# Kernel optimization log

Measured on AMD Instinct MI355X. Metric: run time of the kernel, lower is better.

Reference implementation:

```python
import jax, jax.numpy as jnp
import numpy as np

N = 160000   # total nodes
G = 800      # total graphs (B * 50)
NPG = 200    # nodes per graph
E = 1280000  # total edges (avg degree 8)
B = 16       # proteins
K = 2        # TAGConv hops
IN_F = 31
HID = 64


def setup_inputs() -> dict:
    key = jax.random.key(0)
    ks = jax.random.split(key, 16)
    s = 0.1
    x = jax.random.normal(ks[0], (N, IN_F), jnp.float32)
    src = jax.random.randint(ks[1], (E,), 0, N, jnp.int32)
    dst = jax.random.randint(ks[2], (E,), 0, N, jnp.int32)
    node2graph = jnp.repeat(jnp.arange(G, dtype=jnp.int32), NPG)
    W0 = jax.random.normal(ks[3], (IN_F * (K + 1), HID), jnp.float32) * s
    b0 = jax.random.normal(ks[4], (HID,), jnp.float32) * s
    W1 = jax.random.normal(ks[5], (HID * (K + 1), HID), jnp.float32) * s
    b1 = jax.random.normal(ks[6], (HID,), jnp.float32) * s
    W2 = jax.random.normal(ks[7], (HID * (K + 1), HID), jnp.float32) * s
    b2 = jax.random.normal(ks[8], (HID,), jnp.float32) * s
    W3 = jax.random.normal(ks[9], (HID * (K + 1), HID), jnp.float32) * s
    b3 = jax.random.normal(ks[10], (HID,), jnp.float32) * s
    Wg = jax.random.normal(ks[11], (HID, 1), jnp.float32) * s
    bg = jax.random.normal(ks[12], (1,), jnp.float32) * s
    return dict(x=x, src=src, dst=dst, node2graph=node2graph,
                W0=W0, b0=b0, W1=W1, b1=b1, W2=W2, b2=b2, W3=W3, b3=b3,
                Wg=Wg, bg=bg)


def reference(x, src, dst, node2graph, W0, b0, W1, b1, W2, b2, W3, b3, Wg, bg):
    # symmetric normalization: norm = in_degree^{-1/2}, clamped at 1 (DGL TAGConv)
    deg = jax.ops.segment_sum(jnp.ones((E,), x.dtype), dst, num_segments=N)
    norm = jax.lax.rsqrt(jnp.clip(deg, 1.0))[:, None]  # [N,1]

    def tag_conv(h, W, b):
        hops = [h]
        for _ in range(K):
            h = norm * jax.ops.segment_sum((h * norm)[src], dst, num_segments=N)
            hops.append(h)
        return jnp.concatenate(hops, axis=-1) @ W + b

    h = x
    for W, b in ((W0, b0), (W1, b1), (W2, b2), (W3, b3)):
        h = jax.nn.relu(tag_conv(h, W, b))

    # GlobalAttentionPooling: per-graph softmax over gate logits, weighted sum
    gate = h @ Wg + bg  # [N,1]
    gmax = jax.ops.segment_max(gate, node2graph, num_segments=G)  # [G,1]
    e = jnp.exp(gate - gmax[node2graph])
    z = jax.ops.segment_sum(e, node2graph, num_segments=G)
    alpha = e / z[node2graph]
    readout = jax.ops.segment_sum(alpha * h, node2graph, num_segments=G)  # [G,64]
    return readout.reshape(B, 50, HID)
```

## Files before the change

### kernel.cpp

```cpp
#include <hip/hip_runtime.h>

#define NN 160000
#define NE 1280000
#define NG 800
#define NPGR 200
#define INF_ 31
#define HID 64

#define NBUK 256
#define NPBK 625
#define BCAP 6144
#define CHUNK 8192

typedef unsigned short bfu;
typedef __attribute__((ext_vector_type(8))) short short8;
typedef __attribute__((ext_vector_type(4))) float f32x4;

__device__ inline float bflo(unsigned u) { return __uint_as_float(u << 16); }
__device__ inline float bfhi(unsigned u) { return __uint_as_float(u & 0xffff0000u); }
__device__ inline float bfs(bfu s) { return __uint_as_float(((unsigned)s) << 16); }
__device__ inline unsigned f2bf(float x) {
  unsigned u = __float_as_uint(x);
  return (u + 0x7fffu + ((u >> 16) & 1u)) >> 16;
}
__device__ inline unsigned pack2(float a, float b) {
  return f2bf(a) | (f2bf(b) << 16);
}
__device__ inline void unpack8(uint4 v, float* f) {
  f[0] = bflo(v.x); f[1] = bfhi(v.x);
  f[2] = bflo(v.y); f[3] = bfhi(v.y);
  f[4] = bflo(v.z); f[5] = bfhi(v.z);
  f[6] = bflo(v.w); f[7] = bfhi(v.w);
}

__global__ __launch_bounds__(256) void k_pad(const float* __restrict__ x,
                                             bfu* __restrict__ xb) {
  int i = blockIdx.x * 256 + threadIdx.x;
  int n = i >> 5, f = i & 31;
  float v = (f < INF_) ? x[(size_t)n * INF_ + f] : 0.f;
  xb[i] = (bfu)f2bf(v);
}

__global__ __launch_bounds__(256) void k_wfrag(const float* __restrict__ W,
                                               short* __restrict__ Wf) {
  int idx = blockIdx.x * 256 + threadIdx.x;
  int lane = idx & 63, t = (idx >> 6) & 3, step = idx >> 8;
  int col = t * 16 + (lane & 15);
  int kbase = step * 32 + ((lane >> 4) & 3) * 8;
  short8 o;
#pragma unroll
  for (int j = 0; j < 8; ++j)
    o[j] = (short)f2bf(W[(size_t)(kbase + j) * 64 + col]);
  *reinterpret_cast<short8*>(&Wf[(size_t)idx * 8]) = o;
}

__global__ __launch_bounds__(256) void k_wfrag0(const float* __restrict__ W0,
                                                short* __restrict__ Wf) {
  int idx = blockIdx.x * 256 + threadIdx.x;
  int lane = idx & 63, t = (idx >> 6) & 3, step = idx >> 8;
  int col = t * 16 + (lane & 15);
  int kbase = step * 32 + ((lane >> 4) & 3) * 8;
  short8 o;
#pragma unroll
  for (int j = 0; j < 8; ++j) {
    int r = kbase + j, pp = r >> 5, ir = r & 31;
    float v = (ir < INF_) ? W0[(size_t)(pp * INF_ + ir) * 64 + col] : 0.f;
    o[j] = (short)f2bf(v);
  }
  *reinterpret_cast<short8*>(&Wf[(size_t)idx * 8]) = o;
}

__global__ __launch_bounds__(256) void k_gcinit(int* __restrict__ gcur) {
  gcur[threadIdx.x] = threadIdx.x * BCAP;
}

__global__ __launch_bounds__(256) void k_bucket(const int* __restrict__ src,
    const int* __restrict__ dst, int* __restrict__ gcur,
    uint2* __restrict__ buk, int E) {
  __shared__ uint2 stage[CHUNK];
  __shared__ int cnt[NBUK], gbase[NBUK];
  int tid = threadIdx.x;
  int base = blockIdx.x * CHUNK;
  int nch = min(CHUNK, E - base);
  for (int i = tid; i < NBUK; i += 256) cnt[i] = 0;
  __syncthreads();
  for (int i = tid * 4; i < nch; i += 1024) {
    int4 s4 = *reinterpret_cast<const int4*>(&src[base + i]);
    int4 d4 = *reinterpret_cast<const int4*>(&dst[base + i]);
    stage[i + 0] = make_uint2((unsigned)s4.x, (unsigned)d4.x);
    stage[i + 1] = make_uint2((unsigned)s4.y, (unsigned)d4.y);
    stage[i + 2] = make_uint2((unsigned)s4.z, (unsigned)d4.z);
    stage[i + 3] = make_uint2((unsigned)s4.w, (unsigned)d4.w);
    atomicAdd(&cnt[(unsigned)d4.x / NPBK], 1);
    atomicAdd(&cnt[(unsigned)d4.y / NPBK], 1);
    atomicAdd(&cnt[(unsigned)d4.z / NPBK], 1);
    atomicAdd(&cnt[(unsigned)d4.w / NPBK], 1);
  }
  __syncthreads();
  for (int i = tid; i < NBUK; i += 256) {
    gbase[i] = atomicAdd(&gcur[i], cnt[i]);
    cnt[i] = 0;
  }
  __syncthreads();
  for (int i = tid; i < nch; i += 256) {
    uint2 r = stage[i];
    int b = r.y / NPBK;
    int off = atomicAdd(&cnt[b], 1);
    buk[(size_t)gbase[b] + off] = r;
  }
}

__global__ __launch_bounds__(256) void k_count(const uint2* __restrict__ buk,
    const int* __restrict__ gcur, int* __restrict__ deg,
    int* __restrict__ order) {
  __shared__ int cnt[NPBK];
  __shared__ int h64[64], c64[64];
  int b = blockIdx.x, tid = threadIdx.x;
  int nbase = b * NPBK;
  for (int i = tid; i < NPBK; i += 256) cnt[i] = 0;
  if (tid < 64) h64[tid] = 0;
  __syncthreads();
  int n = gcur[b] - b * BCAP;
  const uint2* __restrict__ bp = buk + (size_t)b * BCAP;
  for (int i = tid; i < n; i += 256) atomicAdd(&cnt[bp[i].y - nbase], 1);
  __syncthreads();
  for (int i = tid; i < NPBK; i += 256) {
    int c = cnt[i];
    deg[nbase + i] = c;
    atomicAdd(&h64[min(c, 63)], 1);
  }
  __syncthreads();
  if (tid == 0) {
    int s = 0;
    for (int k = 0; k < 64; ++k) { c64[k] = s; s += h64[k]; }
  }
  __syncthreads();
  for (int i = tid; i < NPBK; i += 256) {
    int pos = atomicAdd(&c64[min(cnt[i], 63)], 1);
    order[nbase + pos] = nbase + i;
  }
}

__global__ __launch_bounds__(256) void k_bscan(const int* __restrict__ gcur,
                                               int* __restrict__ bktoff) {
  __shared__ int sh[256];
  int tid = threadIdx.x;
  sh[tid] = gcur[tid] - tid * BCAP;
  __syncthreads();
  for (int off = 1; off < 256; off <<= 1) {
    int v = (tid >= off) ? sh[tid - off] : 0;
    __syncthreads();
    sh[tid] += v;
    __syncthreads();
  }
  bktoff[tid] = (tid > 0) ? sh[tid - 1] : 0;
}

__global__ __launch_bounds__(256) void k_scat2(const uint2* __restrict__ buk,
    const int* __restrict__ gcur, const int* __restrict__ bktoff,
    const int* __restrict__ deg, int* __restrict__ rp,
    unsigned* __restrict__ csr) {
  __shared__ int cur[NPBK];
  __shared__ int psum[256];
  int b = blockIdx.x, tid = threadIdx.x;
  int nbase = b * NPBK;
  int i0 = tid * 3;
  int d0 = (i0 + 0 < NPBK) ? deg[nbase + i0 + 0] : 0;
  int d1 = (i0 + 1 < NPBK) ? deg[nbase + i0 + 1] : 0;
  int d2 = (i0 + 2 < NPBK) ? deg[nbase + i0 + 2] : 0;
  psum[tid] = d0 + d1 + d2;
  __syncthreads();
  for (int off = 1; off < 256; off <<= 1) {
    int v = (tid >= off) ? psum[tid - off] : 0;
    __syncthreads();
    psum[tid] += v;
    __syncthreads();
  }
  int excl = bktoff[b] + ((tid > 0) ? psum[tid - 1] : 0);
  if (i0 + 0 < NPBK) { cur[i0 + 0] = excl; rp[nbase + i0 + 0] = excl; excl += d0; }
  if (i0 + 1 < NPBK) { cur[i0 + 1] = excl; rp[nbase + i0 + 1] = excl; excl += d1; }
  if (i0 + 2 < NPBK) { cur[i0 + 2] = excl; rp[nbase + i0 + 2] = excl; excl += d2; }
  if (b == NBUK - 1 && tid == 0) rp[NN] = NE;
  __syncthreads();
  int n = gcur[b] - b * BCAP;
  const uint2* __restrict__ bp = buk + (size_t)b * BCAP;
  for (int i = tid; i < n; i += 256) {
    uint2 r = bp[i];
    int pos = atomicAdd(&cur[r.y - nbase], 1);
    unsigned d = min((unsigned)deg[r.x], 16383u);
    csr[pos] = (d << 18) | r.x;
  }
}

template<int F>
__device__ inline uint4 gather_node(const bfu* __restrict__ hin,
    const unsigned* __restrict__ csr, int beg, int end, int f8) {
  float acc[8] = {0.f, 0.f, 0.f, 0.f, 0.f, 0.f, 0.f, 0.f};
  int e = beg;
  for (; e + 8 <= end; e += 8) {
    unsigned ed[8];
    uint4 v[8];
#pragma unroll
    for (int k = 0; k < 8; ++k) ed[k] = csr[e + k];
#pragma unroll
    for (int k = 0; k < 8; ++k)
      v[k] = *reinterpret_cast<const uint4*>(&hin[(size_t)(ed[k] & 0x3FFFFu) * F + f8]);
#pragma unroll
    for (int k = 0; k < 8; ++k) {
      float f[8];
      unpack8(v[k], f);
      float w = rsqrtf(fmaxf((float)(ed[k] >> 18), 1.0f));
#pragma unroll
      for (int q = 0; q < 8; ++q) acc[q] = fmaf(f[q], w, acc[q]);
    }
  }
  for (; e + 2 <= end; e += 2) {
    unsigned e0 = csr[e], e1 = csr[e + 1];
    uint4 v0 = *reinterpret_cast<const uint4*>(&hin[(size_t)(e0 & 0x3FFFFu) * F + f8]);
    uint4 v1 = *reinterpret_cast<const uint4*>(&hin[(size_t)(e1 & 0x3FFFFu) * F + f8]);
    float f0[8], f1[8];
    unpack8(v0, f0); unpack8(v1, f1);
    float w0 = rsqrtf(fmaxf((float)(e0 >> 18), 1.0f));
    float w1 = rsqrtf(fmaxf((float)(e1 >> 18), 1.0f));
#pragma unroll
    for (int q = 0; q < 8; ++q) {
      acc[q] = fmaf(f0[q], w0, acc[q]);
      acc[q] = fmaf(f1[q], w1, acc[q]);
    }
  }
  if (e < end) {
    unsigned e0 = csr[e];
    uint4 v0 = *reinterpret_cast<const uint4*>(&hin[(size_t)(e0 & 0x3FFFFu) * F + f8]);
    float f0[8];
    unpack8(v0, f0);
    float w0 = rsqrtf(fmaxf((float)(e0 >> 18), 1.0f));
#pragma unroll
    for (int q = 0; q < 8; ++q) acc[q] = fmaf(f0[q], w0, acc[q]);
  }
  float wn = rsqrtf(fmaxf((float)(end - beg), 1.0f));
#pragma unroll
  for (int q = 0; q < 8; ++q) acc[q] *= wn;
  uint4 o;
  o.x = pack2(acc[0], acc[1]);
  o.y = pack2(acc[2], acc[3]);
  o.z = pack2(acc[4], acc[5]);
  o.w = pack2(acc[6], acc[7]);
  return o;
}

template<int F>
__global__ __launch_bounds__(256) void k_gather(const bfu* __restrict__ hin,
    const int* __restrict__ rp, const unsigned* __restrict__ csr,
    const int* __restrict__ order, bfu* __restrict__ hout) {
  constexpr int LPN = F / 8;
  constexpr int NPB = 256 / LPN;
  int slot = threadIdx.x / LPN;
  int f8 = (threadIdx.x % LPN) * 8;
  int nid = order[blockIdx.x * NPB + slot];
  int beg = rp[nid], end = rp[nid + 1];
  uint4 o = gather_node<F>(hin, csr, beg, end, f8);
  *reinterpret_cast<uint4*>(&hout[(size_t)nid * F + f8]) = o;
}

template<int F>
__global__ __launch_bounds__(256) void k_hop2gemm(const bfu* __restrict__ h0,
    const bfu* __restrict__ h1, const int* __restrict__ rp,
    const unsigned* __restrict__ csr, const int* __restrict__ order,
    const short* __restrict__ Wf, const float* __restrict__ bias,
    bfu* __restrict__ outb) {
  constexpr int SPP = F / 32;
  constexpr int LPN = F / 8;
  constexpr int NPR = 256 / LPN;
  constexpr int NFB = F / 8;
  __shared__ uint4 hs[64 * (NFB + 1)];

  int tid = threadIdx.x;
  int nb = blockIdx.x * 64;

#pragma unroll
  for (int round = 0; round < 64 / NPR; ++round) {
    int slot = round * NPR + tid / LPN;
    int f8 = tid % LPN;
    int nid = order[nb + slot];
    int beg = rp[nid], end = rp[nid + 1];
    uint4 o = gather_node<F>(h1, csr, beg, end, f8 * 8);
    hs[slot * (NFB + 1) + f8] = o;
  }
  __syncthreads();

  int wave = tid >> 6, lane = tid & 63;
  int quad = lane >> 4, l15 = lane & 15;
  int aslot = wave * 16 + l15;
  int anid = order[nb + aslot];

  f32x4 acc[4] = {{0.f,0.f,0.f,0.f}, {0.f,0.f,0.f,0.f},
                  {0.f,0.f,0.f,0.f}, {0.f,0.f,0.f,0.f}};
  const bfu* parts[2] = {h0, h1};
#pragma unroll
  for (int p = 0; p < 2; ++p) {
    const bfu* __restrict__ P = parts[p] + (size_t)anid * F + quad * 8;
#pragma unroll
    for (int s = 0; s < SPP; ++s) {
      short8 a = *reinterpret_cast<const short8*>(P + s * 32);
      int step = p * SPP + s;
      const short* __restrict__ wb = Wf + ((size_t)step * 4 * 64 + lane) * 8;
#pragma unroll
      for (int t = 0; t < 4; ++t) {
        short8 b = *reinterpret_cast<const short8*>(wb + (size_t)t * 64 * 8);
        acc[t] = __builtin_amdgcn_mfma_f32_16x16x32_bf16(a, b, acc[t], 0, 0, 0);
      }
    }
  }
#pragma unroll
  for (int s = 0; s < SPP; ++s) {
    short8 a = *reinterpret_cast<const short8*>(&hs[aslot * (NFB + 1) + s * 4 + quad]);
    int step = 2 * SPP + s;
    const short* __restrict__ wb = Wf + ((size_t)step * 4 * 64 + lane) * 8;
#pragma unroll
    for (int t = 0; t < 4; ++t) {
      short8 b = *reinterpret_cast<const short8*>(wb + (size_t)t * 64 * 8);
      acc[t] = __builtin_amdgcn_mfma_f32_16x16x32_bf16(a, b, acc[t], 0, 0, 0);
    }
  }
#pragma unroll
  for (int t = 0; t < 4; ++t) {
    int col = t * 16 + l15;
    float bj = bias[col];
#pragma unroll
    for (int r = 0; r < 4; ++r) {
      int node = order[nb + wave * 16 + quad * 4 + r];
      float v = fmaxf(acc[t][r] + bj, 0.f);
      outb[(size_t)node * 64 + col] = (bfu)f2bf(v);
    }
  }
}

__global__ __launch_bounds__(256) void k_pool(const bfu* __restrict__ h,
    const float* __restrict__ Wg, const float* __restrict__ bg,
    float* __restrict__ out) {
  __shared__ uint4 hsl[NPGR * 8];
  __shared__ float sgate[NPGR];
  __shared__ float sred[256];
  __shared__ float spart[4][64];
  int g = blockIdx.x;
  int tid = threadIdx.x;
  int lane = tid & 63, w = tid >> 6;
  const uint4* __restrict__ hg4 = reinterpret_cast<const uint4*>(
      h + (size_t)g * NPGR * HID);
  for (int i = tid; i < NPGR * 8; i += 256) hsl[i] = hg4[i];
  __syncthreads();
  const bfu* hsb = reinterpret_cast<const bfu*>(hsl);
  float wgt = Wg[lane];

  for (int n = w; n < NPGR; n += 4) {
    float v = bfs(hsb[n * HID + lane]) * wgt;
    for (int off = 32; off > 0; off >>= 1) v += __shfl_down(v, off, 64);
    if (lane == 0) sgate[n] = v + bg[0];
  }
  __syncthreads();

  float m = -INFINITY;
  for (int n = tid; n < NPGR; n += 256) m = fmaxf(m, sgate[n]);
  sred[tid] = m;
  __syncthreads();
  for (int s = 128; s > 0; s >>= 1) {
    if (tid < s) sred[tid] = fmaxf(sred[tid], sred[tid + s]);
    __syncthreads();
  }
  float gmax = sred[0];
  __syncthreads();

  float zp = 0.f;
  for (int n = tid; n < NPGR; n += 256) {
    float e = expf(sgate[n] - gmax);
    sgate[n] = e;
    zp += e;
  }
  sred[tid] = zp;
  __syncthreads();
  for (int s = 128; s > 0; s >>= 1) {
    if (tid < s) sred[tid] += sred[tid + s];
    __syncthreads();
  }
  float z = sred[0];
  __syncthreads();

  float acc = 0.f;
  for (int n = w; n < NPGR; n += 4)
    acc += sgate[n] * bfs(hsb[n * HID + lane]);
  spart[w][lane] = acc;
  __syncthreads();
  if (w == 0) {
    float t = spart[0][lane] + spart[1][lane] + spart[2][lane] + spart[3][lane];
    out[(size_t)g * HID + lane] = t / z;
  }
}

extern "C" void kernel_launch(void* const* d_in, const int* in_sizes, int n_in,
                              void* d_out, int out_size, void* d_ws, size_t ws_size,
                              hipStream_t stream) {
  const float* x   = (const float*)d_in[0];
  const int*   src = (const int*)d_in[1];
  const int*   dst = (const int*)d_in[2];
  const float* W0 = (const float*)d_in[4];
  const float* b0 = (const float*)d_in[5];
  const float* W1 = (const float*)d_in[6];
  const float* b1 = (const float*)d_in[7];
  const float* W2 = (const float*)d_in[8];
  const float* b2 = (const float*)d_in[9];
  const float* W3 = (const float*)d_in[10];
  const float* b3 = (const float*)d_in[11];
  const float* Wg = (const float*)d_in[12];
  const float* bg = (const float*)d_in[13];
  float* out = (float*)d_out;

  const int N = NN, E = NE;

  char* p = (char*)d_ws;
  unsigned* csr = (unsigned*)p;      p += sizeof(unsigned) * (size_t)E;
  int* deg     = (int*)p;            p += sizeof(int) * (size_t)N;
  int* rp      = (int*)p;            p += sizeof(int) * (size_t)(N + 4);
  int* order   = (int*)p;            p += sizeof(int) * (size_t)N;
  int* gcur    = (int*)p;            p += sizeof(int) * NBUK;
  int* bktoff  = (int*)p;            p += sizeof(int) * NBUK;
  short* Wf0   = (short*)p;          p += sizeof(short) * 768 * 8;
  short* Wf1   = (short*)p;          p += sizeof(short) * 1536 * 8;
  short* Wf2   = (short*)p;          p += sizeof(short) * 1536 * 8;
  short* Wf3   = (short*)p;          p += sizeof(short) * 1536 * 8;
  bfu* xb      = (bfu*)p;            p += sizeof(bfu) * (size_t)N * 32;
  bfu* h1b     = (bfu*)p;            p += sizeof(bfu) * (size_t)N * HID;
  bfu* hAb     = (bfu*)p;            p += sizeof(bfu) * (size_t)N * HID;
  bfu* hBb     = (bfu*)p;            p += sizeof(bfu) * (size_t)N * HID;
  uint2* buk   = (uint2*)p;
  p += sizeof(uint2) * (size_t)NBUK * BCAP;

  k_gcinit<<<1, NBUK, 0, stream>>>(gcur);
  k_bucket<<<(E + CHUNK - 1) / CHUNK, 256, 0, stream>>>(src, dst, gcur, buk, E);
  k_count<<<NBUK, 256, 0, stream>>>(buk, gcur, deg, order);
  k_bscan<<<1, NBUK, 0, stream>>>(gcur, bktoff);
  k_scat2<<<NBUK, 256, 0, stream>>>(buk, gcur, bktoff, deg, rp, csr);

  k_pad<<<(N * 32) / 256, 256, 0, stream>>>(x, xb);
  k_wfrag0<<<3, 256, 0, stream>>>(W0, Wf0);
  k_wfrag<<<6, 256, 0, stream>>>(W1, Wf1);
  k_wfrag<<<6, 256, 0, stream>>>(W2, Wf2);
  k_wfrag<<<6, 256, 0, stream>>>(W3, Wf3);

  k_gather<32><<<N / 64, 256, 0, stream>>>(xb, rp, csr, order, h1b);
  k_hop2gemm<32><<<N / 64, 256, 0, stream>>>(xb, h1b, rp, csr, order,
                                             Wf0, b0, hAb);

  const short* Wfs[3] = {Wf1, Wf2, Wf3};
  const float* bs[3] = {b1, b2, b3};
  bfu* hin = hAb;
  bfu* hout = hBb;
  for (int l = 0; l < 3; ++l) {
    k_gather<64><<<N / 32, 256, 0, stream>>>(hin, rp, csr, order, h1b);
    k_hop2gemm<64><<<N / 64, 256, 0, stream>>>(hin, h1b, rp, csr, order,
                                               Wfs[l], bs[l], hout);
    bfu* t = hin; hin = hout; hout = t;
  }

  k_pool<<<NG, 256, 0, stream>>>(hin, Wg, bg, out);
}
```

Measured before the change: 579.6 us.

## Sort nodes by id within degree windows and raise occupancy bounds

```diff
diff --git a/kernel.cpp b/kernel.cpp
--- a/kernel.cpp
+++ b/kernel.cpp
@@ -7,9 +7,9 @@
 #define INF_ 31
 #define HID 64
 
-#define NBUK 256
-#define NPBK 625
-#define BCAP 6144
+#define NBUK 250
+#define NPBK 640
+#define BCAP 6400
 #define CHUNK 8192
 
 typedef unsigned short bfu;
@@ -71,7 +71,8 @@
 }
 
 __global__ __launch_bounds__(256) void k_gcinit(int* __restrict__ gcur) {
-  gcur[threadIdx.x] = threadIdx.x * BCAP;
+  int tid = threadIdx.x;
+  if (tid < NBUK) gcur[tid] = tid * BCAP;
 }
 
 __global__ __launch_bounds__(256) void k_bucket(const int* __restrict__ src,
@@ -114,6 +115,7 @@
     const int* __restrict__ gcur, int* __restrict__ deg,
     int* __restrict__ order) {
   __shared__ int cnt[NPBK];
+  __shared__ int sord[NPBK];
   __shared__ int h64[64], c64[64];
   int b = blockIdx.x, tid = threadIdx.x;
   int nbase = b * NPBK;
@@ -137,15 +139,32 @@
   __syncthreads();
   for (int i = tid; i < NPBK; i += 256) {
     int pos = atomicAdd(&c64[min(cnt[i], 63)], 1);
-    order[nbase + pos] = nbase + i;
-  }
+    sord[pos] = nbase + i;
+  }
+  __syncthreads();
+  for (int k = 2; k <= 64; k <<= 1) {
+    for (int j = k >> 1; j > 0; j >>= 1) {
+      for (int g = tid; g < NPBK; g += 256) {
+        int i = g & 63, w = g >> 6;
+        int l = i ^ j;
+        if (l > i) {
+          int gi = w * 64 + i, gl = w * 64 + l;
+          int a = sord[gi], c = sord[gl];
+          bool up = ((i & k) == 0);
+          if ((a > c) == up) { sord[gi] = c; sord[gl] = a; }
+        }
+      }
+      __syncthreads();
+    }
+  }
+  for (int i = tid; i < NPBK; i += 256) order[nbase + i] = sord[i];
 }
 
 __global__ __launch_bounds__(256) void k_bscan(const int* __restrict__ gcur,
                                                int* __restrict__ bktoff) {
   __shared__ int sh[256];
   int tid = threadIdx.x;
-  sh[tid] = gcur[tid] - tid * BCAP;
+  sh[tid] = (tid < NBUK) ? (gcur[tid] - tid * BCAP) : 0;
   __syncthreads();
   for (int off = 1; off < 256; off <<= 1) {
     int v = (tid >= off) ? sh[tid - off] : 0;
@@ -153,7 +172,7 @@
     sh[tid] += v;
     __syncthreads();
   }
-  bktoff[tid] = (tid > 0) ? sh[tid - 1] : 0;
+  if (tid < NBUK) bktoff[tid] = (tid > 0) ? sh[tid - 1] : 0;
 }
 
 __global__ __launch_bounds__(256) void k_scat2(const uint2* __restrict__ buk,
@@ -249,7 +268,7 @@
 }
 
 template<int F>
-__global__ __launch_bounds__(256) void k_gather(const bfu* __restrict__ hin,
+__global__ __launch_bounds__(256, 8) void k_gather(const bfu* __restrict__ hin,
     const int* __restrict__ rp, const unsigned* __restrict__ csr,
     const int* __restrict__ order, bfu* __restrict__ hout) {
   constexpr int LPN = F / 8;
@@ -263,7 +282,7 @@
 }
 
 template<int F>
-__global__ __launch_bounds__(256) void k_hop2gemm(const bfu* __restrict__ h0,
+__global__ __launch_bounds__(256, 8) void k_hop2gemm(const bfu* __restrict__ h0,
     const bfu* __restrict__ h1, const int* __restrict__ rp,
     const unsigned* __restrict__ csr, const int* __restrict__ order,
     const short* __restrict__ Wf, const float* __restrict__ bias,
@@ -421,8 +440,8 @@
   int* deg     = (int*)p;            p += sizeof(int) * (size_t)N;
   int* rp      = (int*)p;            p += sizeof(int) * (size_t)(N + 4);
   int* order   = (int*)p;            p += sizeof(int) * (size_t)N;
-  int* gcur    = (int*)p;            p += sizeof(int) * NBUK;
-  int* bktoff  = (int*)p;            p += sizeof(int) * NBUK;
+  int* gcur    = (int*)p;            p += sizeof(int) * NBUK + 24;
+  int* bktoff  = (int*)p;            p += sizeof(int) * NBUK + 24;
   short* Wf0   = (short*)p;          p += sizeof(short) * 768 * 8;
   short* Wf1   = (short*)p;          p += sizeof(short) * 1536 * 8;
   short* Wf2   = (short*)p;          p += sizeof(short) * 1536 * 8;
@@ -434,10 +453,10 @@
   uint2* buk   = (uint2*)p;
   p += sizeof(uint2) * (size_t)NBUK * BCAP;
 
-  k_gcinit<<<1, NBUK, 0, stream>>>(gcur);
+  k_gcinit<<<1, 256, 0, stream>>>(gcur);
   k_bucket<<<(E + CHUNK - 1) / CHUNK, 256, 0, stream>>>(src, dst, gcur, buk, E);
   k_count<<<NBUK, 256, 0, stream>>>(buk, gcur, deg, order);
-  k_bscan<<<1, NBUK, 0, stream>>>(gcur, bktoff);
+  k_bscan<<<1, 256, 0, stream>>>(gcur, bktoff);
   k_scat2<<<NBUK, 256, 0, stream>>>(buk, gcur, bktoff, deg, rp, csr);
 
   k_pad<<<(N * 32) / 256, 256, 0, stream>>>(x, xb);
```

Measured after the change: 637.4 us. 10.0% more time.
